# Kernel tuning notes

Hardware: AMD Instinct MI355X
Metric: run time of the kernel (lower is better)

Reference implementation:

```python
import jax, jax.numpy as jnp
import numpy as np

N, L, S = 2, 3000, 3000
C = 256          # in_depth
H = 256          # hidden_depth
FC = 8           # heads_count
SC_HID = H // FC # per-head dim of projected features
SCALE = (C // FC) ** 0.5  # torch code uses sc = in_depth // heads_count for scaling


def setup_inputs() -> dict:
    key = jax.random.key(0)
    ks = jax.random.split(key, 7)
    x0 = jax.random.normal(ks[0], (N, L, C), jnp.float32)
    x1 = jax.random.normal(ks[1], (N, S, C), jnp.float32)
    mask = jax.random.bernoulli(ks[2], 0.9, (N, L, S))
    W_proj = jax.random.normal(ks[3], (C, 2 * H), jnp.float32) / np.sqrt(C).astype(np.float32)
    b_proj = jax.random.normal(ks[4], (2 * H,), jnp.float32) * 0.01
    W_merge = jax.random.normal(ks[5], (H, C), jnp.float32) / np.sqrt(H).astype(np.float32)
    b_merge = jax.random.normal(ks[6], (C,), jnp.float32) * 0.01
    return {"x0": x0, "x1": x1, "mask": mask,
            "W_proj": W_proj, "b_proj": b_proj,
            "W_merge": W_merge, "b_merge": b_merge}


def _split_heads(x, W_proj, b_proj):
    # x: [n, t, C] -> proj [n, t, 2H] -> (qk, v) each [n, fc, t, sc]
    n, t, _ = x.shape
    p = (x @ W_proj + b_proj).reshape(n, t, 2, FC, SC_HID)  # layout (k fc sc)
    qk = jnp.transpose(p[:, :, 0], (0, 2, 1, 3))
    v = jnp.transpose(p[:, :, 1], (0, 2, 1, 3))
    return qk, v


def reference(x0, x1, mask, W_proj, b_proj, W_merge, b_merge):
    q0, v0 = _split_heads(x0, W_proj, b_proj)  # [n, f, l, d]
    q1, v1 = _split_heads(x1, W_proj, b_proj)  # [n, f, s, d]

    sim = jnp.einsum('nfld,nfsd->nfls', q0, q1)            # full score matrix
    sim = jnp.where(mask[:, None], sim, -jnp.inf) / SCALE  # mask then scale (as in torch)

    a01 = jnp.nan_to_num(jax.nn.softmax(sim, axis=3))  # rows over s
    a10 = jnp.nan_to_num(jax.nn.softmax(sim, axis=2))  # rows over l (== softmax(sim^T, -1))

    m0 = jnp.einsum('nfls,nfsd->nfld', a01, v1)  # [n, f, l, d]
    m1 = jnp.einsum('nfls,nfld->nfsd', a10, v0)  # [n, f, s, d]

    m0 = jnp.transpose(m0, (0, 2, 1, 3)).reshape(m0.shape[0], L, H) @ W_merge + b_merge
    m1 = jnp.transpose(m1, (0, 2, 1, 3)).reshape(m1.shape[0], S, H) @ W_merge + b_merge
    return m0, m1
```

## Files before the change

kernel.cpp:

```cpp
#include <hip/hip_runtime.h>
#include <cstdint>
#include <cstddef>

typedef unsigned int u32;
typedef unsigned short u16;
typedef uint8_t u8;
typedef unsigned long long u64;

constexpr int kNB = 2, kL = 3000, kS = 3000, kC = 256, kH = 256, kFC = 8, kD = 32;
constexpr int kTP = 3008;
constexpr int kMW = 48;
constexpr float kQSC = 0.5050097568f;

typedef __attribute__((ext_vector_type(8))) short short8;
typedef __attribute__((ext_vector_type(4))) float f32x4;

__device__ __forceinline__ u16 f2bf(float f) {
  u32 u = __float_as_uint(f);
  u += 0x7FFFu + ((u >> 16) & 1u);
  return (u16)(u >> 16);
}
__device__ __forceinline__ float bf2f(u16 h) { return __uint_as_float(((u32)h) << 16); }
__device__ __forceinline__ f32x4 mfma16(short8 a, short8 b, f32x4 c) {
  return __builtin_amdgcn_mfma_f32_16x16x32_bf16(a, b, c, 0, 0, 0);
}
__device__ __forceinline__ u32 pk2(float a, float b) {
  return (__float_as_uint(a) >> 16) | (__float_as_uint(b) & 0xFFFF0000u);
}
__device__ __forceinline__ float truncbf(float a) {
  return __uint_as_float(__float_as_uint(a) & 0xFFFF0000u);
}
__device__ __forceinline__ u32 bytes_nz(u32 w) {
  return ((w & 0xFFu) ? 1u : 0u) | (((w >> 8) & 0xFFu) ? 2u : 0u)
       | (((w >> 16) & 0xFFu) ? 4u : 0u) | ((w >> 24) ? 8u : 0u);
}
__device__ __forceinline__ u32 h2_nz(u32 w) {
  return ((w & 0xFFFFu) ? 1u : 0u) | ((w >> 16) ? 2u : 0u);
}

__device__ __forceinline__ u32 detect_mf_block(const u8* __restrict__ mraw,
                                               int tid, int* cnt) {
  if (tid < 8) cnt[tid] = 0;
  __syncthreads();
  uint4 mv = ((const uint4*)mraw)[tid];
  u32 wds[4] = {mv.x, mv.y, mv.z, mv.w};
  int l1[4] = {0,0,0,0}; int l3f1 = 0, l3c = 0;
#pragma unroll
  for (int k = 0; k < 4; ++k) {
    u32 wv = wds[k];
#pragma unroll
    for (int j = 0; j < 4; ++j) {
      u32 b = (wv >> (8 * j)) & 0xFFu;
      l1[j] += (b == 1u);
      if (j == 1) l3f1 += (b == 0x3Fu);
      if (j & 1) l3c += (b == 0x3Cu);
    }
  }
  if (l1[0]) atomicAdd(&cnt[0], l1[0]);
  if (l1[1]) atomicAdd(&cnt[1], l1[1]);
  if (l1[2]) atomicAdd(&cnt[2], l1[2]);
  if (l1[3]) atomicAdd(&cnt[3], l1[3]);
  if (l3f1)  atomicAdd(&cnt[4], l3f1);
  if (l3c)   atomicAdd(&cnt[5], l3c);
  __syncthreads();
  u32 mf;
  if (cnt[1] + cnt[2] + cnt[3] > 64) mf = 0;
  else if (cnt[0] > 64)              mf = 2;
  else if (cnt[4] > 64)              mf = 1;
  else if (cnt[5] > 64)              mf = 4;
  else                               mf = 3;
  return mf;
}
__device__ __forceinline__ u32 detect_f2_block(const u8* __restrict__ xraw,
                                               int tid, int* cnt) {
  if (tid == 0) cnt[0] = 0;
  __syncthreads();
  uint4 xv = ((const uint4*)xraw)[tid];
  u32 wds[4] = {xv.x, xv.y, xv.z, xv.w};
  int lex = 0;
#pragma unroll
  for (int k = 0; k < 4; ++k) {
    u32 b = (wds[k] >> 8) & 0x7Fu;
    lex += (b >= 0x3Eu && b <= 0x40u);
  }
  if (lex) atomicAdd(&cnt[0], lex);
  __syncthreads();
  return (cnt[0] > 300) ? 0u : 1u;
}

constexpr size_t SZ_Q   = (size_t)kNB * kFC * kTP * kD * 2;
constexpr size_t SZ_MH  = (size_t)kNB * kTP * kH * 2;
constexpr size_t SZ_XB  = (size_t)kNB * kL * kC * 2;
constexpr size_t SZ_MKB = (size_t)kNB * kMW * kTP * 8;
constexpr size_t OFF_Q0 = 256;
constexpr size_t OFF_Q1 = OFF_Q0 + SZ_Q;
constexpr size_t OFF_V0 = OFF_Q1 + SZ_Q;
constexpr size_t OFF_V1 = OFF_V0 + SZ_Q;
constexpr size_t OFF_M0 = OFF_V1 + SZ_Q;
constexpr size_t OFF_M1 = OFF_M0 + SZ_MH;
constexpr size_t OFF_WT = OFF_M1 + SZ_MH;
constexpr size_t OFF_WM = OFF_WT + (size_t)2 * kH * kC * 2;
constexpr size_t OFF_X0 = OFF_WM + (size_t)kC * kH * 2;
constexpr size_t OFF_X1 = OFF_X0 + SZ_XB;
constexpr size_t OFF_MKB  = OFF_X1 + SZ_XB;
constexpr size_t OFF_MKBT = OFF_MKB + SZ_MKB;

constexpr int NB_MASK = 47 * 47 * 2;
constexpr int NB_CVT  = 3000;
constexpr int NB_WT   = 2 * kH + kC;

__global__ __launch_bounds__(256) void k_prep(const void* __restrict__ mraw,
                                              const void* __restrict__ x0,
                                              const void* __restrict__ x1,
                                              const void* __restrict__ Wp,
                                              const void* __restrict__ Wm,
                                              u64* __restrict__ mkb, u64* __restrict__ mkbt,
                                              u16* __restrict__ xb0, u16* __restrict__ xb1,
                                              u16* __restrict__ WT, u16* __restrict__ WmT) {
  const int bx = blockIdx.x, tid = threadIdx.x;
  __shared__ int dcnt[8];
  if (bx < NB_MASK) {
    const u32 mf = detect_mf_block((const u8*)mraw, tid, dcnt);
    const int n = bx / 2209, r2 = bx % 2209;
    const int l0 = (r2 / 47) * 64, s0 = (r2 % 47) * 64;
    __shared__ u16 tb[64][4];
    {
      const int row = tid >> 2, sg = (tid & 3) * 16;
      const int l = l0 + row;
      u32 bits = 0;
      if (l < kL) {
        const size_t base = ((size_t)n * kL + l) * kS + s0 + sg;
        const bool full = (s0 + sg + 16 <= kS);
        if (mf == 3) {
          if (full) {
            const float4* p = (const float4*)(((const float*)mraw) + base);
            float4 a = p[0], b = p[1], c = p[2], d = p[3];
            bits = (u32)(a.x != 0.f)        | ((u32)(a.y != 0.f) << 1)
                 | ((u32)(a.z != 0.f) << 2) | ((u32)(a.w != 0.f) << 3)
                 | ((u32)(b.x != 0.f) << 4) | ((u32)(b.y != 0.f) << 5)
                 | ((u32)(b.z != 0.f) << 6) | ((u32)(b.w != 0.f) << 7)
                 | ((u32)(c.x != 0.f) << 8) | ((u32)(c.y != 0.f) << 9)
                 | ((u32)(c.z != 0.f) << 10)| ((u32)(c.w != 0.f) << 11)
                 | ((u32)(d.x != 0.f) << 12)| ((u32)(d.y != 0.f) << 13)
                 | ((u32)(d.z != 0.f) << 14)| ((u32)(d.w != 0.f) << 15);
          } else {
            for (int i = 0; i < 16; ++i)
              if (s0 + sg + i < kS && ((const float*)mraw)[base + i] != 0.f) bits |= 1u << i;
          }
        } else if (mf == 2) {
          if (full) {
            const uint4* p = (const uint4*)(((const u32*)mraw) + base);
            uint4 a = p[0], b = p[1], c = p[2], d = p[3];
            bits = (u32)(a.x != 0)        | ((u32)(a.y != 0) << 1)
                 | ((u32)(a.z != 0) << 2) | ((u32)(a.w != 0) << 3)
                 | ((u32)(b.x != 0) << 4) | ((u32)(b.y != 0) << 5)
                 | ((u32)(b.z != 0) << 6) | ((u32)(b.w != 0) << 7)
                 | ((u32)(c.x != 0) << 8) | ((u32)(c.y != 0) << 9)
                 | ((u32)(c.z != 0) << 10)| ((u32)(c.w != 0) << 11)
                 | ((u32)(d.x != 0) << 12)| ((u32)(d.y != 0) << 13)
                 | ((u32)(d.z != 0) << 14)| ((u32)(d.w != 0) << 15);
          } else {
            for (int i = 0; i < 16; ++i)
              if (s0 + sg + i < kS && ((const u32*)mraw)[base + i]) bits |= 1u << i;
          }
        } else if (mf == 0) {
          if (full) {
            const u8* m8 = (const u8*)mraw + base;
            uint2 a = *(const uint2*)(m8);
            uint2 b = *(const uint2*)(m8 + 8);
            bits = bytes_nz(a.x) | (bytes_nz(a.y) << 4)
                 | (bytes_nz(b.x) << 8) | (bytes_nz(b.y) << 12);
          } else {
            for (int i = 0; i < 16; ++i)
              if (s0 + sg + i < kS && ((const u8*)mraw)[base + i]) bits |= 1u << i;
          }
        } else {
          if (full) {
            const u16* m16 = (const u16*)mraw + base;
            uint4 a = *(const uint4*)(m16);
            uint4 b = *(const uint4*)(m16 + 8);
            bits = h2_nz(a.x) | (h2_nz(a.y) << 2) | (h2_nz(a.z) << 4) | (h2_nz(a.w) << 6)
                 | (h2_nz(b.x) << 8) | (h2_nz(b.y) << 10)
                 | (h2_nz(b.z) << 12) | (h2_nz(b.w) << 14);
          } else {
            for (int i = 0; i < 16; ++i)
              if (s0 + sg + i < kS && ((const u16*)mraw)[base + i]) bits |= 1u << i;
          }
        }
      }
      tb[row][tid & 3] = (u16)bits;
    }
    __syncthreads();
    const int w = tid >> 6, lane = tid & 63;
    for (int k = 0; k < 16; ++k) {
      const int ro = w * 16 + k;
      u32 b1 = (tb[ro][lane >> 4] >> (lane & 15)) & 1;
      u64 word = __ballot((int)b1);
      if (lane == 0) mkb[((size_t)n * kMW + (s0 >> 6)) * kTP + l0 + ro] = word;
      u32 b2 = (tb[lane][ro >> 4] >> (ro & 15)) & 1;
      u64 wordt = __ballot((int)b2);
      if (lane == 0) mkbt[((size_t)n * kMW + (l0 >> 6)) * kTP + s0 + ro] = wordt;
    }
  } else if (bx < NB_MASK + NB_CVT) {
    const u32 f2 = detect_f2_block((const u8*)x0, tid, dcnt);
    const int b2 = bx - NB_MASK;
    const void* X = (b2 >= 1500) ? x1 : x0;
    u16* B = (b2 >= 1500) ? xb1 : xb0;
    const int i = (b2 % 1500) * 256 + tid;
    if (f2 == 0) {
      ((uint2*)B)[i] = ((const uint2*)X)[i];
    } else {
      float4 v = ((const float4*)X)[i];
      uint2 o;
      o.x = (u32)f2bf(v.x) | ((u32)f2bf(v.y) << 16);
      o.y = (u32)f2bf(v.z) | ((u32)f2bf(v.w) << 16);
      ((uint2*)B)[i] = o;
    }
  } else {
    const u32 f2 = detect_f2_block((const u8*)x0, tid, dcnt);
    const int b = bx - NB_MASK - NB_CVT, k = tid;
    if (b < 2 * kH) {
      int col = b;
      u16 v = (f2 == 0) ? ((const u16*)Wp)[(size_t)k * (2 * kH) + col]
                        : f2bf(((const float*)Wp)[(size_t)k * (2 * kH) + col]);
      WT[(size_t)col * kC + k] = v;
    } else {
      int col = b - 2 * kH;
      u16 v = (f2 == 0) ? ((const u16*)Wm)[(size_t)k * kC + col]
                        : f2bf(((const float*)Wm)[(size_t)k * kC + col]);
      WmT[(size_t)col * kH + k] = v;
    }
  }
}

__global__ __launch_bounds__(256) void k_proj(const u16* __restrict__ xb0,
                                              const u16* __restrict__ xb1,
                                              const u16* __restrict__ WT,
                                              const void* __restrict__ bias,
                                              const void* __restrict__ x0raw,
                                              u16* __restrict__ q0, u16* __restrict__ v0t,
                                              u16* __restrict__ q1, u16* __restrict__ v1t) {
  __shared__ int dcnt[8];
  const int tid = threadIdx.x;
  const u32 f2 = detect_f2_block((const u8*)x0raw, tid, dcnt);
  const int z = blockIdx.z;
  const u16* X = z ? xb1 : xb0;
  u16* Q = z ? q1 : q0;
  u16* V = z ? v1t : v0t;
  const int w = tid >> 6, lane = tid & 63;
  const int quad = lane >> 4, c16 = lane & 15;
  const int rb = blockIdx.x, cb = blockIdx.y;

  __align__(16) __shared__ u16 sB[64 * 264];
  {
    const u16* wp = WT + (size_t)(cb * 64 + (tid >> 2)) * kC + (tid & 3) * 64;
    u16* sp = sB + (tid >> 2) * 264 + (tid & 3) * 64;
#pragma unroll
    for (int i = 0; i < 8; ++i) *(uint4*)(sp + i * 8) = *(const uint4*)(wp + i * 8);
  }
  __syncthreads();

  const int arow = rb * 64 + w * 16 + c16;
  const u16* ap = X + (size_t)arow * kC + quad * 8;
  f32x4 acc[4];
#pragma unroll
  for (int cg = 0; cg < 4; ++cg) acc[cg] = f32x4{0.f,0.f,0.f,0.f};
#pragma unroll
  for (int k0 = 0; k0 < 8; ++k0) {
    short8 a = *(const short8*)(ap + k0 * 32);
#pragma unroll
    for (int cg = 0; cg < 4; ++cg) {
      short8 b = *(const short8*)(sB + (cg * 16 + c16) * 264 + k0 * 32 + quad * 8);
      acc[cg] = mfma16(a, b, acc[cg]);
    }
  }

  const int row0 = rb * 64 + w * 16 + quad * 4;
  if (row0 < 6000) {
    const int n = (row0 >= kL) ? 1 : 0;
    const int t0 = row0 - n * kL;
#pragma unroll
    for (int cg = 0; cg < 4; ++cg) {
      const int c = cb * 64 + cg * 16 + c16;
      float bb = (f2 == 0) ? bf2f(((const u16*)bias)[c]) : ((const float*)bias)[c];
      if (c < kH) {
        int ff = c >> 5, d = c & 31;
        u16* qp = Q + ((size_t)(n * kFC + ff) * kTP + t0) * kD + d;
#pragma unroll
        for (int r = 0; r < 4; ++r) qp[(size_t)r * kD] = f2bf((acc[cg][r] + bb) * kQSC);
      } else {
        int cc = c - kH;
        int ff = cc >> 5, d = cc & 31;
        uint2 o;
        o.x = (u32)f2bf(acc[cg][0] + bb) | ((u32)f2bf(acc[cg][1] + bb) << 16);
        o.y = (u32)f2bf(acc[cg][2] + bb) | ((u32)f2bf(acc[cg][3] + bb) << 16);
        *(uint2*)(V + ((size_t)(n * kFC + ff) * kD + d) * kTP + t0) = o;
      }
    }
  }
}

__global__ __launch_bounds__(256) void k_flash(const u16* __restrict__ q0,
                                               const u16* __restrict__ q1,
                                               const u16* __restrict__ v0t,
                                               const u16* __restrict__ v1t,
                                               const u64* __restrict__ mkb,
                                               const u64* __restrict__ mkbt,
                                               u16* __restrict__ m0h, u16* __restrict__ m1h) {
  const int z = blockIdx.z;
  const u16* QA = z ? q1 : q0;
  const u16* QB = z ? q0 : q1;
  const u16* VT = z ? v0t : v1t;
  const u64* MB = z ? mkbt : mkb;
  u16* MO = z ? m1h : m0h;

  const int nf = blockIdx.y, n = nf >> 3, f = nf & 7;
  const int tid = threadIdx.x, w = tid >> 6, lane = tid & 63;
  const int quad = lane >> 4, c16 = lane & 15;

  __align__(16) __shared__ u16 sPall[4 * 4704];
  u16* sP = sPall + w * 4704;

  const u16* qa = QA + (size_t)(n * kFC + f) * kTP * kD;
  const u16* qb = QB + (size_t)(n * kFC + f) * kTP * kD;
  const u16* vt = VT + (size_t)(n * kFC + f) * kD * kTP;
  const u64* mb = MB + (size_t)n * kMW * kTP;

  const int l0 = blockIdx.x * 64;

  short8 af[4];
#pragma unroll
  for (int g = 0; g < 4; ++g) {
    const int ra = l0 + g * 16 + c16;
    af[g] = *(const short8*)(qa + (size_t)ra * kD + quad * 8);
  }

  f32x4 acc[4][2];
  float pSum[4];
#pragma unroll
  for (int g = 0; g < 4; ++g) {
    acc[g][0] = f32x4{0.f,0.f,0.f,0.f};
    acc[g][1] = f32x4{0.f,0.f,0.f,0.f};
    pSum[g] = 0.f;
  }

  u64 mword = mb[(size_t)w * kTP + l0 + lane];
  short8 aq0, aq1, aq2, aq3;
  {
    const u16* qbase = qb + (size_t)(w * 64 + c16) * kD + quad * 8;
    aq0 = *(const short8*)(qbase);
    aq1 = *(const short8*)(qbase + (size_t)16 * kD);
    aq2 = *(const short8*)(qbase + (size_t)32 * kD);
    aq3 = *(const short8*)(qbase + (size_t)48 * kD);
  }

#pragma unroll 1
  for (int jc = w; jc < 47; jc += 4) {
    const int j0 = jc * 64;
    const u16* vb = vt + (size_t)c16 * kTP + j0 + quad * 8;
    short8 bv00 = *(const short8*)(vb);
    short8 bv01 = *(const short8*)(vb + (size_t)16 * kTP);
    short8 bv10 = *(const short8*)(vb + 32);
    short8 bv11 = *(const short8*)(vb + (size_t)16 * kTP + 32);

    const u32 mlo = (u32)mword, mhi = (u32)(mword >> 32);

#pragma unroll
    for (int g = 0; g < 4; ++g) {
      const u32 lo = (u32)__shfl((int)mlo, g * 16 + c16);
      const u32 hi = (u32)__shfl((int)mhi, g * 16 + c16);
      float ps = 0.f;
#pragma unroll
      for (int t = 0; t < 4; ++t) {
        short8 aq = (t == 0) ? aq0 : (t == 1) ? aq1 : (t == 2) ? aq2 : aq3;
        f32x4 zz = {0.f,0.f,0.f,0.f};
        f32x4 s = mfma16(aq, af[g], zz);
        const u32 hh = (t & 2) ? hi : lo;
        const int base = (t & 1) * 16 + quad * 4;
        float p0 = ((hh >> (base + 0)) & 1) ? __builtin_amdgcn_exp2f(s[0]) : 0.f;
        float p1 = ((hh >> (base + 1)) & 1) ? __builtin_amdgcn_exp2f(s[1]) : 0.f;
        float p2 = ((hh >> (base + 2)) & 1) ? __builtin_amdgcn_exp2f(s[2]) : 0.f;
        float p3 = ((hh >> (base + 3)) & 1) ? __builtin_amdgcn_exp2f(s[3]) : 0.f;
        ps += (truncbf(p0) + truncbf(p1)) + (truncbf(p2) + truncbf(p3));
        uint2 pw; pw.x = pk2(p0, p1); pw.y = pk2(p2, p3);
        *(uint2*)(sP + (g * 16 + c16) * 72 + t * 16 + quad * 4) = pw;
      }
      pSum[g] += ps;
    }

    {
      int jn = jc + 4;
      const int jl = (jn < 47) ? jn : w;
      mword = mb[(size_t)jl * kTP + l0 + lane];
      const u16* qn = qb + (size_t)(jl * 64 + c16) * kD + quad * 8;
      aq0 = *(const short8*)(qn);
      aq1 = *(const short8*)(qn + (size_t)16 * kD);
      aq2 = *(const short8*)(qn + (size_t)32 * kD);
      aq3 = *(const short8*)(qn + (size_t)48 * kD);
    }

#pragma unroll
    for (int g = 0; g < 4; ++g) {
      short8 ap0 = *(const short8*)(sP + (g * 16 + c16) * 72 + quad * 8);
      short8 ap1 = *(const short8*)(sP + (g * 16 + c16) * 72 + 32 + quad * 8);
      acc[g][0] = mfma16(ap0, bv00, acc[g][0]);
      acc[g][1] = mfma16(ap0, bv01, acc[g][1]);
      acc[g][0] = mfma16(ap1, bv10, acc[g][0]);
      acc[g][1] = mfma16(ap1, bv11, acc[g][1]);
    }
  }

#pragma unroll
  for (int g = 0; g < 4; ++g) {
    float s = pSum[g];
    s += __shfl_xor(s, 16);
    s += __shfl_xor(s, 32);
    pSum[g] = s;
  }

  __syncthreads();
  float* buf = (float*)sPall;
  if (w > 0) {
    const int rbase = (w - 1) * 2304;
#pragma unroll
    for (int g = 0; g < 4; ++g) {
#pragma unroll
      for (int r = 0; r < 4; ++r) {
        buf[rbase + (g * 9 + r)     * 64 + lane] = acc[g][0][r];
        buf[rbase + (g * 9 + 4 + r) * 64 + lane] = acc[g][1][r];
      }
      buf[rbase + (g * 9 + 8) * 64 + lane] = pSum[g];
    }
  }
  __syncthreads();
  if (w == 0) {
#pragma unroll
    for (int g = 0; g < 4; ++g) {
      float lsum = pSum[g];
#pragma unroll
      for (int ww = 0; ww < 3; ++ww) lsum += buf[ww * 2304 + (g * 9 + 8) * 64 + lane];
#pragma unroll
      for (int r = 0; r < 4; ++r) {
        float n0 = acc[g][0][r], n1 = acc[g][1][r];
#pragma unroll
        for (int ww = 0; ww < 3; ++ww) {
          n0 += buf[ww * 2304 + (g * 9 + r)     * 64 + lane];
          n1 += buf[ww * 2304 + (g * 9 + 4 + r) * 64 + lane];
        }
        float ls = __shfl(lsum, quad * 4 + r);
        float rd = (ls > 0.f) ? (1.f / ls) : 0.f;
        int lrow = l0 + g * 16 + quad * 4 + r;
        if (lrow < kL) {
          size_t basep = ((size_t)n * kTP + lrow) * kH + f * kD;
          MO[basep + c16]      = f2bf(n0 * rd);
          MO[basep + 16 + c16] = f2bf(n1 * rd);
        }
      }
    }
  }
}

__global__ __launch_bounds__(256) void k_merge(const u16* __restrict__ m0h,
                                               const u16* __restrict__ m1h,
                                               const u16* __restrict__ WmT,
                                               const void* __restrict__ bias,
                                               const void* __restrict__ x0raw,
                                               void* __restrict__ out) {
  __shared__ int dcnt[8];
  const int tid = threadIdx.x;
  const u32 f2 = detect_f2_block((const u8*)x0raw, tid, dcnt);
  const int z = blockIdx.z;
  const u16* A = z ? m1h : m0h;
  const int w = tid >> 6, lane = tid & 63;
  const int quad = lane >> 4, c16 = lane & 15;
  const int rb = blockIdx.x, cb = blockIdx.y;

  __align__(16) __shared__ u16 sB[64 * 264];
  {
    const u16* wp = WmT + (size_t)(cb * 64 + (tid >> 2)) * kH + (tid & 3) * 64;
    u16* sp = sB + (tid >> 2) * 264 + (tid & 3) * 64;
#pragma unroll
    for (int i = 0; i < 8; ++i) *(uint4*)(sp + i * 8) = *(const uint4*)(wp + i * 8);
  }
  __syncthreads();

  const int arow = rb * 64 + w * 16 + c16;
  const u16* ap = A + (size_t)arow * kH + quad * 8;
  f32x4 acc[4];
#pragma unroll
  for (int cg = 0; cg < 4; ++cg) acc[cg] = f32x4{0.f,0.f,0.f,0.f};
#pragma unroll
  for (int k0 = 0; k0 < 8; ++k0) {
    short8 a = *(const short8*)(ap + k0 * 32);
#pragma unroll
    for (int cg = 0; cg < 4; ++cg) {
      short8 b = *(const short8*)(sB + (cg * 16 + c16) * 264 + k0 * 32 + quad * 8);
      acc[cg] = mfma16(a, b, acc[cg]);
    }
  }

  const int row0 = rb * 64 + w * 16 + quad * 4;
  const int n = (row0 >= kTP) ? 1 : 0;
  const int t0 = row0 - n * kTP;
  const size_t obase = (size_t)z * ((size_t)kNB * kL * kC);
#pragma unroll
  for (int cg = 0; cg < 4; ++cg) {
    const int c = cb * 64 + cg * 16 + c16;
    float bb = (f2 == 0) ? bf2f(((const u16*)bias)[c]) : ((const float*)bias)[c];
#pragma unroll
    for (int r = 0; r < 4; ++r) {
      const int t = t0 + r;
      if (t < kL) {
        size_t oi = obase + ((size_t)n * kL + t) * kC + c;
        float v = acc[cg][r] + bb;
        if (f2 == 0) ((u16*)out)[oi] = f2bf(v);
        else         ((float*)out)[oi] = v;
      }
    }
  }
}

extern "C" void kernel_launch(void* const* d_in, const int* in_sizes, int n_in,
                              void* d_out, int out_size, void* d_ws, size_t ws_size,
                              hipStream_t stream) {
  (void)in_sizes; (void)n_in; (void)out_size; (void)ws_size;
  u8* ws = (u8*)d_ws;
  u16* q0  = (u16*)(ws + OFF_Q0);
  u16* q1  = (u16*)(ws + OFF_Q1);
  u16* v0t = (u16*)(ws + OFF_V0);
  u16* v1t = (u16*)(ws + OFF_V1);
  u16* m0h = (u16*)(ws + OFF_M0);
  u16* m1h = (u16*)(ws + OFF_M1);
  u16* WT  = (u16*)(ws + OFF_WT);
  u16* WmT = (u16*)(ws + OFF_WM);
  u16* xb0 = (u16*)(ws + OFF_X0);
  u16* xb1 = (u16*)(ws + OFF_X1);
  u64* mkb  = (u64*)(ws + OFF_MKB);
  u64* mkbt = (u64*)(ws + OFF_MKBT);

  const void* x0 = d_in[0];
  const void* x1 = d_in[1];
  const void* mraw = d_in[2];
  const void* Wp = d_in[3];
  const void* bp = d_in[4];
  const void* Wm = d_in[5];
  const void* bm = d_in[6];

  k_prep<<<dim3(NB_MASK + NB_CVT + NB_WT), 256, 0, stream>>>(
      mraw, x0, x1, Wp, Wm, mkb, mkbt, xb0, xb1, WT, WmT);
  k_proj<<<dim3(94, 8, 2), 256, 0, stream>>>(xb0, xb1, WT, bp, x0, q0, v0t, q1, v1t);
  k_flash<<<dim3(47, 16, 2), 256, 0, stream>>>(q0, q1, v0t, v1t, mkb, mkbt, m0h, m1h);
  k_merge<<<dim3(94, 4, 2), 256, 0, stream>>>(m0h, m1h, WmT, bm, x0, d_out);
}
```

Measured before the change: 258.4 us.

## Fuse four kernels into one persistent kernel with grid-wide barriers

Replaces the four separate launches (prep, projection, flash attention, merge) with a single persistent kernel of 512 blocks. Each block loops over the virtual block indices of every stage, and atomic-counter grid barriers in the workspace separate the stages. This removes the launch gaps and tail idle time between kernels. In exchange it adds an extra memset, spin-wait barriers, and a fixed grid size that may cut occupancy or load balance for the flash stage; correctness also depends on all 512 blocks being resident at once.

```diff
diff --git a/kernel.cpp b/kernel.cpp
--- a/kernel.cpp
+++ b/kernel.cpp
@@ -10,6 +10,7 @@
 constexpr int kNB = 2, kL = 3000, kS = 3000, kC = 256, kH = 256, kFC = 8, kD = 32;
 constexpr int kTP = 3008;
 constexpr int kMW = 48;
+constexpr int kNBLK = 512;
 constexpr float kQSC = 0.5050097568f;
 
 typedef __attribute__((ext_vector_type(8))) short short8;
@@ -27,65 +28,12 @@
 __device__ __forceinline__ u32 pk2(float a, float b) {
   return (__float_as_uint(a) >> 16) | (__float_as_uint(b) & 0xFFFF0000u);
 }
-__device__ __forceinline__ float truncbf(float a) {
-  return __uint_as_float(__float_as_uint(a) & 0xFFFF0000u);
-}
 __device__ __forceinline__ u32 bytes_nz(u32 w) {
   return ((w & 0xFFu) ? 1u : 0u) | (((w >> 8) & 0xFFu) ? 2u : 0u)
        | (((w >> 16) & 0xFFu) ? 4u : 0u) | ((w >> 24) ? 8u : 0u);
 }
 __device__ __forceinline__ u32 h2_nz(u32 w) {
   return ((w & 0xFFFFu) ? 1u : 0u) | ((w >> 16) ? 2u : 0u);
-}
-
-__device__ __forceinline__ u32 detect_mf_block(const u8* __restrict__ mraw,
-                                               int tid, int* cnt) {
-  if (tid < 8) cnt[tid] = 0;
-  __syncthreads();
-  uint4 mv = ((const uint4*)mraw)[tid];
-  u32 wds[4] = {mv.x, mv.y, mv.z, mv.w};
-  int l1[4] = {0,0,0,0}; int l3f1 = 0, l3c = 0;
-#pragma unroll
-  for (int k = 0; k < 4; ++k) {
-    u32 wv = wds[k];
-#pragma unroll
-    for (int j = 0; j < 4; ++j) {
-      u32 b = (wv >> (8 * j)) & 0xFFu;
-      l1[j] += (b == 1u);
-      if (j == 1) l3f1 += (b == 0x3Fu);
-      if (j & 1) l3c += (b == 0x3Cu);
-    }
-  }
-  if (l1[0]) atomicAdd(&cnt[0], l1[0]);
-  if (l1[1]) atomicAdd(&cnt[1], l1[1]);
-  if (l1[2]) atomicAdd(&cnt[2], l1[2]);
-  if (l1[3]) atomicAdd(&cnt[3], l1[3]);
-  if (l3f1)  atomicAdd(&cnt[4], l3f1);
-  if (l3c)   atomicAdd(&cnt[5], l3c);
-  __syncthreads();
-  u32 mf;
-  if (cnt[1] + cnt[2] + cnt[3] > 64) mf = 0;
-  else if (cnt[0] > 64)              mf = 2;
-  else if (cnt[4] > 64)              mf = 1;
-  else if (cnt[5] > 64)              mf = 4;
-  else                               mf = 3;
-  return mf;
-}
-__device__ __forceinline__ u32 detect_f2_block(const u8* __restrict__ xraw,
-                                               int tid, int* cnt) {
-  if (tid == 0) cnt[0] = 0;
-  __syncthreads();
-  uint4 xv = ((const uint4*)xraw)[tid];
-  u32 wds[4] = {xv.x, xv.y, xv.z, xv.w};
-  int lex = 0;
-#pragma unroll
-  for (int k = 0; k < 4; ++k) {
-    u32 b = (wds[k] >> 8) & 0x7Fu;
-    lex += (b >= 0x3Eu && b <= 0x40u);
-  }
-  if (lex) atomicAdd(&cnt[0], lex);
-  __syncthreads();
-  return (cnt[0] > 300) ? 0u : 1u;
 }
 
 constexpr size_t SZ_Q   = (size_t)kNB * kFC * kTP * kD * 2;
@@ -105,418 +53,466 @@
 constexpr size_t OFF_MKB  = OFF_X1 + SZ_XB;
 constexpr size_t OFF_MKBT = OFF_MKB + SZ_MKB;
 
+__device__ __forceinline__ u32 detect_mf_block(const u8* __restrict__ mraw,
+                                               int tid, int* cnt) {
+  if (tid < 8) cnt[tid] = 0;
+  __syncthreads();
+  uint4 mv = ((const uint4*)mraw)[tid];
+  u32 wds[4] = {mv.x, mv.y, mv.z, mv.w};
+  int l1[4] = {0,0,0,0}; int l3f1 = 0, l3c = 0;
+#pragma unroll
+  for (int k = 0; k < 4; ++k) {
+    u32 wv = wds[k];
+#pragma unroll
+    for (int j = 0; j < 4; ++j) {
+      u32 b = (wv >> (8 * j)) & 0xFFu;
+      l1[j] += (b == 1u);
+      if (j == 1) l3f1 += (b == 0x3Fu);
+      if (j & 1) l3c += (b == 0x3Cu);
+    }
+  }
+  if (l1[0]) atomicAdd(&cnt[0], l1[0]);
+  if (l1[1]) atomicAdd(&cnt[1], l1[1]);
+  if (l1[2]) atomicAdd(&cnt[2], l1[2]);
+  if (l1[3]) atomicAdd(&cnt[3], l1[3]);
+  if (l3f1)  atomicAdd(&cnt[4], l3f1);
+  if (l3c)   atomicAdd(&cnt[5], l3c);
+  __syncthreads();
+  u32 mf;
+  if (cnt[1] + cnt[2] + cnt[3] > 64) mf = 0;
+  else if (cnt[0] > 64)              mf = 2;
+  else if (cnt[4] > 64)              mf = 1;
+  else if (cnt[5] > 64)              mf = 4;
+  else                               mf = 3;
+  return mf;
+}
+__device__ __forceinline__ u32 detect_f2_block(const u8* __restrict__ xraw,
+                                               int tid, int* cnt) {
+  __syncthreads();
+  if (tid == 0) cnt[6] = 0;
+  __syncthreads();
+  uint4 xv = ((const uint4*)xraw)[tid];
+  u32 wds[4] = {xv.x, xv.y, xv.z, xv.w};
+  int lex = 0;
+#pragma unroll
+  for (int k = 0; k < 4; ++k) {
+    u32 b = (wds[k] >> 8) & 0x7Fu;
+    lex += (b >= 0x3Eu && b <= 0x40u);
+  }
+  if (lex) atomicAdd(&cnt[6], lex);
+  __syncthreads();
+  return (cnt[6] > 300) ? 0u : 1u;
+}
+
+__device__ __forceinline__ void gridbar(u32* bar, int idx, int tid) {
+  __syncthreads();
+  if (tid == 0) {
+    __threadfence();
+    __hip_atomic_fetch_add(&bar[idx], 1u, __ATOMIC_ACQ_REL, __HIP_MEMORY_SCOPE_AGENT);
+    while (__hip_atomic_load(&bar[idx], __ATOMIC_ACQUIRE, __HIP_MEMORY_SCOPE_AGENT)
+           < (u32)kNBLK) { __builtin_amdgcn_s_sleep(2); }
+    __threadfence();
+  }
+  __syncthreads();
+}
+
 constexpr int NB_MASK = 47 * 47 * 2;
 constexpr int NB_CVT  = 3000;
 constexpr int NB_WT   = 2 * kH + kC;
-
-__global__ __launch_bounds__(256) void k_prep(const void* __restrict__ mraw,
-                                              const void* __restrict__ x0,
-                                              const void* __restrict__ x1,
-                                              const void* __restrict__ Wp,
-                                              const void* __restrict__ Wm,
-                                              u64* __restrict__ mkb, u64* __restrict__ mkbt,
-                                              u16* __restrict__ xb0, u16* __restrict__ xb1,
-                                              u16* __restrict__ WT, u16* __restrict__ WmT) {
-  const int bx = blockIdx.x, tid = threadIdx.x;
+constexpr int NB_PREP = NB_MASK + NB_CVT + NB_WT;
+constexpr int NB_PROJ = 94 * 8 * 2;
+constexpr int NB_FLSH = 47 * 16 * 2;
+constexpr int NB_MRG  = 94 * 4 * 2;
+
+__global__ __launch_bounds__(256, 2) void k_all(const void* __restrict__ mraw,
+                                                const void* __restrict__ x0,
+                                                const void* __restrict__ x1,
+                                                const void* __restrict__ Wp,
+                                                const void* __restrict__ Wm,
+                                                const void* __restrict__ bp,
+                                                const void* __restrict__ bm,
+                                                u8* __restrict__ ws,
+                                                void* __restrict__ out) {
+  u32* bar  = (u32*)ws;
+  u16* q0   = (u16*)(ws + OFF_Q0);
+  u16* q1   = (u16*)(ws + OFF_Q1);
+  u16* v0t  = (u16*)(ws + OFF_V0);
+  u16* v1t  = (u16*)(ws + OFF_V1);
+  u16* m0h  = (u16*)(ws + OFF_M0);
+  u16* m1h  = (u16*)(ws + OFF_M1);
+  u16* WT   = (u16*)(ws + OFF_WT);
+  u16* WmT  = (u16*)(ws + OFF_WM);
+  u16* xb0  = (u16*)(ws + OFF_X0);
+  u16* xb1  = (u16*)(ws + OFF_X1);
+  u64* mkb  = (u64*)(ws + OFF_MKB);
+  u64* mkbt = (u64*)(ws + OFF_MKBT);
+
+  const int bid = blockIdx.x, tid = threadIdx.x;
+  const int w = tid >> 6, lane = tid & 63;
+  const int quad = lane >> 4, c16 = lane & 15;
+
   __shared__ int dcnt[8];
-  if (bx < NB_MASK) {
-    const u32 mf = detect_mf_block((const u8*)mraw, tid, dcnt);
-    const int n = bx / 2209, r2 = bx % 2209;
-    const int l0 = (r2 / 47) * 64, s0 = (r2 % 47) * 64;
-    __shared__ u16 tb[64][4];
-    {
-      const int row = tid >> 2, sg = (tid & 3) * 16;
-      const int l = l0 + row;
-      u32 bits = 0;
-      if (l < kL) {
-        const size_t base = ((size_t)n * kL + l) * kS + s0 + sg;
-        const bool full = (s0 + sg + 16 <= kS);
-        if (mf == 3) {
-          if (full) {
-            const float4* p = (const float4*)(((const float*)mraw) + base);
-            float4 a = p[0], b = p[1], c = p[2], d = p[3];
-            bits = (u32)(a.x != 0.f)        | ((u32)(a.y != 0.f) << 1)
-                 | ((u32)(a.z != 0.f) << 2) | ((u32)(a.w != 0.f) << 3)
-                 | ((u32)(b.x != 0.f) << 4) | ((u32)(b.y != 0.f) << 5)
-                 | ((u32)(b.z != 0.f) << 6) | ((u32)(b.w != 0.f) << 7)
-                 | ((u32)(c.x != 0.f) << 8) | ((u32)(c.y != 0.f) << 9)
-                 | ((u32)(c.z != 0.f) << 10)| ((u32)(c.w != 0.f) << 11)
-                 | ((u32)(d.x != 0.f) << 12)| ((u32)(d.y != 0.f) << 13)
-                 | ((u32)(d.z != 0.f) << 14)| ((u32)(d.w != 0.f) << 15);
+  __align__(16) __shared__ u16 smem[4 * 4704];
+
+  const u32 mf = detect_mf_block((const u8*)mraw, tid, dcnt);
+  const u32 f2 = detect_f2_block((const u8*)x0, tid, dcnt);
+
+  for (int vb = bid; vb < NB_PREP; vb += kNBLK) {
+    if (vb < NB_MASK) {
+      const int n = vb / 2209, r2 = vb % 2209;
+      const int l0 = (r2 / 47) * 64, s0 = (r2 % 47) * 64;
+      u16 (*tb)[4] = (u16(*)[4])smem;
+      {
+        const int row = tid >> 2, sg = (tid & 3) * 16;
+        const int l = l0 + row;
+        u32 bits = 0;
+        if (l < kL) {
+          const size_t base = ((size_t)n * kL + l) * kS + s0 + sg;
+          const bool full = (s0 + sg + 16 <= kS);
+          if (mf == 3) {
+            if (full) {
+              const float4* p = (const float4*)(((const float*)mraw) + base);
+              float4 a = p[0], b = p[1], c = p[2], d = p[3];
+              bits = (u32)(a.x != 0.f)        | ((u32)(a.y != 0.f) << 1)
+                   | ((u32)(a.z != 0.f) << 2) | ((u32)(a.w != 0.f) << 3)
+                   | ((u32)(b.x != 0.f) << 4) | ((u32)(b.y != 0.f) << 5)
+                   | ((u32)(b.z != 0.f) << 6) | ((u32)(b.w != 0.f) << 7)
+                   | ((u32)(c.x != 0.f) << 8) | ((u32)(c.y != 0.f) << 9)
+                   | ((u32)(c.z != 0.f) << 10)| ((u32)(c.w != 0.f) << 11)
+                   | ((u32)(d.x != 0.f) << 12)| ((u32)(d.y != 0.f) << 13)
+                   | ((u32)(d.z != 0.f) << 14)| ((u32)(d.w != 0.f) << 15);
+            } else {
+              for (int i = 0; i < 16; ++i)
+                if (s0 + sg + i < kS && ((const float*)mraw)[base + i] != 0.f) bits |= 1u << i;
+            }
+          } else if (mf == 2) {
+            if (full) {
+              const uint4* p = (const uint4*)(((const u32*)mraw) + base);
+              uint4 a = p[0], b = p[1], c = p[2], d = p[3];
+              bits = (u32)(a.x != 0)        | ((u32)(a.y != 0) << 1)
+                   | ((u32)(a.z != 0) << 2) | ((u32)(a.w != 0) << 3)
+                   | ((u32)(b.x != 0) << 4) | ((u32)(b.y != 0) << 5)
+                   | ((u32)(b.z != 0) << 6) | ((u32)(b.w != 0) << 7)
+                   | ((u32)(c.x != 0) << 8) | ((u32)(c.y != 0) << 9)
+                   | ((u32)(c.z != 0) << 10)| ((u32)(c.w != 0) << 11)
+                   | ((u32)(d.x != 0) << 12)| ((u32)(d.y != 0) << 13)
+                   | ((u32)(d.z != 0) << 14)| ((u32)(d.w != 0) << 15);
+            } else {
+              for (int i = 0; i < 16; ++i)
+                if (s0 + sg + i < kS && ((const u32*)mraw)[base + i]) bits |= 1u << i;
+            }
+          } else if (mf == 0) {
+            if (full) {
+              const u8* m8 = (const u8*)mraw + base;
+              uint2 a = *(const uint2*)(m8);
+              uint2 b = *(const uint2*)(m8 + 8);
+              bits = bytes_nz(a.x) | (bytes_nz(a.y) << 4)
+                   | (bytes_nz(b.x) << 8) | (bytes_nz(b.y) << 12);
+            } else {
+              for (int i = 0; i < 16; ++i)
+                if (s0 + sg + i < kS && ((const u8*)mraw)[base + i]) bits |= 1u << i;
+            }
           } else {
-            for (int i = 0; i < 16; ++i)
-              if (s0 + sg + i < kS && ((const float*)mraw)[base + i] != 0.f) bits |= 1u << i;
-          }
-        } else if (mf == 2) {
-          if (full) {
-            const uint4* p = (const uint4*)(((const u32*)mraw) + base);
-            uint4 a = p[0], b = p[1], c = p[2], d = p[3];
-            bits = (u32)(a.x != 0)        | ((u32)(a.y != 0) << 1)
-                 | ((u32)(a.z != 0) << 2) | ((u32)(a.w != 0) << 3)
-                 | ((u32)(b.x != 0) << 4) | ((u32)(b.y != 0) << 5)
-                 | ((u32)(b.z != 0) << 6) | ((u32)(b.w != 0) << 7)
-                 | ((u32)(c.x != 0) << 8) | ((u32)(c.y != 0) << 9)
-                 | ((u32)(c.z != 0) << 10)| ((u32)(c.w != 0) << 11)
-                 | ((u32)(d.x != 0) << 12)| ((u32)(d.y != 0) << 13)
-                 | ((u32)(d.z != 0) << 14)| ((u32)(d.w != 0) << 15);
-          } else {
-            for (int i = 0; i < 16; ++i)
-              if (s0 + sg + i < kS && ((const u32*)mraw)[base + i]) bits |= 1u << i;
-          }
-        } else if (mf == 0) {
-          if (full) {
-            const u8* m8 = (const u8*)mraw + base;
-            uint2 a = *(const uint2*)(m8);
-            uint2 b = *(const uint2*)(m8 + 8);
-            bits = bytes_nz(a.x) | (bytes_nz(a.y) << 4)
-                 | (bytes_nz(b.x) << 8) | (bytes_nz(b.y) << 12);
-          } else {
-            for (int i = 0; i < 16; ++i)
-              if (s0 + sg + i < kS && ((const u8*)mraw)[base + i]) bits |= 1u << i;
-          }
-        } else {
-          if (full) {
-            const u16* m16 = (const u16*)mraw + base;
-            uint4 a = *(const uint4*)(m16);
-            uint4 b = *(const uint4*)(m16 + 8);
-            bits = h2_nz(a.x) | (h2_nz(a.y) << 2) | (h2_nz(a.z) << 4) | (h2_nz(a.w) << 6)
-                 | (h2_nz(b.x) << 8) | (h2_nz(b.y) << 10)
-                 | (h2_nz(b.z) << 12) | (h2_nz(b.w) << 14);
-          } else {
-            for (int i = 0; i < 16; ++i)
-              if (s0 + sg + i < kS && ((const u16*)mraw)[base + i]) bits |= 1u << i;
+            if (full) {
+              const u16* m16 = (const u16*)mraw + base;
+              uint4 a = *(const uint4*)(m16);
+              uint4 b = *(const uint4*)(m16 + 8);
+              bits = h2_nz(a.x) | (h2_nz(a.y) << 2) | (h2_nz(a.z) << 4) | (h2_nz(a.w) << 6)
+                   | (h2_nz(b.x) << 8) | (h2_nz(b.y) << 10)
+                   | (h2_nz(b.z) << 12) | (h2_nz(b.w) << 14);
+            } else {
+              for (int i = 0; i < 16; ++i)
+                if (s0 + sg + i < kS && ((const u16*)mraw)[base + i]) bits |= 1u << i;
+            }
           }
         }
-      }
-      tb[row][tid & 3] = (u16)bits;
-    }
-    __syncthreads();
-    const int w = tid >> 6, lane = tid & 63;
-    for (int k = 0; k < 16; ++k) {
-      const int ro = w * 16 + k;
-      u32 b1 = (tb[ro][lane >> 4] >> (lane & 15)) & 1;
-      u64 word = __ballot((int)b1);
-      if (lane == 0) mkb[((size_t)n * kMW + (s0 >> 6)) * kTP + l0 + ro] = word;
-      u32 b2 = (tb[lane][ro >> 4] >> (ro & 15)) & 1;
-      u64 wordt = __ballot((int)b2);
-      if (lane == 0) mkbt[((size_t)n * kMW + (l0 >> 6)) * kTP + s0 + ro] = wordt;
-    }
-  } else if (bx < NB_MASK + NB_CVT) {
-    const u32 f2 = detect_f2_block((const u8*)x0, tid, dcnt);
-    const int b2 = bx - NB_MASK;
-    const void* X = (b2 >= 1500) ? x1 : x0;
-    u16* B = (b2 >= 1500) ? xb1 : xb0;
-    const int i = (b2 % 1500) * 256 + tid;
-    if (f2 == 0) {
-      ((uint2*)B)[i] = ((const uint2*)X)[i];
+        tb[row][tid & 3] = (u16)bits;
+      }
+      __syncthreads();
+      for (int k = 0; k < 16; ++k) {
+        const int ro = w * 16 + k;
+        u32 b1 = (tb[ro][lane >> 4] >> (lane & 15)) & 1;
+        u64 word = __ballot((int)b1);
+        if (lane == 0) mkb[((size_t)n * kMW + (s0 >> 6)) * kTP + l0 + ro] = word;
+        u32 b2 = (tb[lane][ro >> 4] >> (ro & 15)) & 1;
+        u64 wordt = __ballot((int)b2);
+        if (lane == 0) mkbt[((size_t)n * kMW + (l0 >> 6)) * kTP + s0 + ro] = wordt;
+      }
+      __syncthreads();
+    } else if (vb < NB_MASK + NB_CVT) {
+      const int b2 = vb - NB_MASK;
+      const void* X = (b2 >= 1500) ? x1 : x0;
+      u16* B = (b2 >= 1500) ? xb1 : xb0;
+      const int i = (b2 % 1500) * 256 + tid;
+      if (f2 == 0) {
+        ((uint2*)B)[i] = ((const uint2*)X)[i];
+      } else {
+        float4 v = ((const float4*)X)[i];
+        uint2 o;
+        o.x = (u32)f2bf(v.x) | ((u32)f2bf(v.y) << 16);
+        o.y = (u32)f2bf(v.z) | ((u32)f2bf(v.w) << 16);
+        ((uint2*)B)[i] = o;
+      }
     } else {
-      float4 v = ((const float4*)X)[i];
-      uint2 o;
-      o.x = (u32)f2bf(v.x) | ((u32)f2bf(v.y) << 16);
-      o.y = (u32)f2bf(v.z) | ((u32)f2bf(v.w) << 16);
-      ((uint2*)B)[i] = o;
-    }
-  } else {
-    const u32 f2 = detect_f2_block((const u8*)x0, tid, dcnt);
-    const int b = bx - NB_MASK - NB_CVT, k = tid;
-    if (b < 2 * kH) {
-      int col = b;
-      u16 v = (f2 == 0) ? ((const u16*)Wp)[(size_t)k * (2 * kH) + col]
-                        : f2bf(((const float*)Wp)[(size_t)k * (2 * kH) + col]);
-      WT[(size_t)col * kC + k] = v;
-    } else {
-      int col = b - 2 * kH;
-      u16 v = (f2 == 0) ? ((const u16*)Wm)[(size_t)k * kC + col]
-                        : f2bf(((const float*)Wm)[(size_t)k * kC + col]);
-      WmT[(size_t)col * kH + k] = v;
-    }
-  }
-}
-
-__global__ __launch_bounds__(256) void k_proj(const u16* __restrict__ xb0,
-                                              const u16* __restrict__ xb1,
-                                              const u16* __restrict__ WT,
-                                              const void* __restrict__ bias,
-                                              const void* __restrict__ x0raw,
-                                              u16* __restrict__ q0, u16* __restrict__ v0t,
-                                              u16* __restrict__ q1, u16* __restrict__ v1t) {
-  __shared__ int dcnt[8];
-  const int tid = threadIdx.x;
-  const u32 f2 = detect_f2_block((const u8*)x0raw, tid, dcnt);
-  const int z = blockIdx.z;
-  const u16* X = z ? xb1 : xb0;
-  u16* Q = z ? q1 : q0;
-  u16* V = z ? v1t : v0t;
-  const int w = tid >> 6, lane = tid & 63;
-  const int quad = lane >> 4, c16 = lane & 15;
-  const int rb = blockIdx.x, cb = blockIdx.y;
-
-  __align__(16) __shared__ u16 sB[64 * 264];
-  {
-    const u16* wp = WT + (size_t)(cb * 64 + (tid >> 2)) * kC + (tid & 3) * 64;
-    u16* sp = sB + (tid >> 2) * 264 + (tid & 3) * 64;
-#pragma unroll
-    for (int i = 0; i < 8; ++i) *(uint4*)(sp + i * 8) = *(const uint4*)(wp + i * 8);
-  }
-  __syncthreads();
-
-  const int arow = rb * 64 + w * 16 + c16;
-  const u16* ap = X + (size_t)arow * kC + quad * 8;
-  f32x4 acc[4];
-#pragma unroll
-  for (int cg = 0; cg < 4; ++cg) acc[cg] = f32x4{0.f,0.f,0.f,0.f};
-#pragma unroll
-  for (int k0 = 0; k0 < 8; ++k0) {
-    short8 a = *(const short8*)(ap + k0 * 32);
-#pragma unroll
-    for (int cg = 0; cg < 4; ++cg) {
-      short8 b = *(const short8*)(sB + (cg * 16 + c16) * 264 + k0 * 32 + quad * 8);
-      acc[cg] = mfma16(a, b, acc[cg]);
-    }
-  }
-
-  const int row0 = rb * 64 + w * 16 + quad * 4;
-  if (row0 < 6000) {
-    const int n = (row0 >= kL) ? 1 : 0;
-    const int t0 = row0 - n * kL;
+      const int b = vb - NB_MASK - NB_CVT, k = tid;
+      if (b < 2 * kH) {
+        int col = b;
+        u16 v = (f2 == 0) ? ((const u16*)Wp)[(size_t)k * (2 * kH) + col]
+                          : f2bf(((const float*)Wp)[(size_t)k * (2 * kH) + col]);
+        WT[(size_t)col * kC + k] = v;
+      } else {
+        int col = b - 2 * kH;
+        u16 v = (f2 == 0) ? ((const u16*)Wm)[(size_t)k * kC + col]
+                          : f2bf(((const float*)Wm)[(size_t)k * kC + col]);
+        WmT[(size_t)col * kH + k] = v;
+      }
+    }
+  }
+  gridbar(bar, 0, tid);
+
+  for (int vb = bid; vb < NB_PROJ; vb += kNBLK) {
+    const int rb = vb % 94, cb = (vb / 94) % 8, z = vb / 752;
+    const u16* X = z ? xb1 : xb0;
+    u16* Q = z ? q1 : q0;
+    u16* V = z ? v1t : v0t;
+    u16* sB = smem;
+    {
+      const u16* wp = WT + (size_t)(cb * 64 + (tid >> 2)) * kC + (tid & 3) * 64;
+      u16* sp = sB + (tid >> 2) * 264 + (tid & 3) * 64;
+#pragma unroll
+      for (int i = 0; i < 8; ++i) *(uint4*)(sp + i * 8) = *(const uint4*)(wp + i * 8);
+    }
+    __syncthreads();
+
+    const int arow = rb * 64 + w * 16 + c16;
+    const u16* ap = X + (size_t)arow * kC + quad * 8;
+    f32x4 acc[4];
+#pragma unroll
+    for (int cg = 0; cg < 4; ++cg) acc[cg] = f32x4{0.f,0.f,0.f,0.f};
+#pragma unroll
+    for (int k0 = 0; k0 < 8; ++k0) {
+      short8 a = *(const short8*)(ap + k0 * 32);
+#pragma unroll
+      for (int cg = 0; cg < 4; ++cg) {
+        short8 b = *(const short8*)(sB + (cg * 16 + c16) * 264 + k0 * 32 + quad * 8);
+        acc[cg] = mfma16(a, b, acc[cg]);
+      }
+    }
+
+    const int row0 = rb * 64 + w * 16 + quad * 4;
+    if (row0 < 2 * kL) {
+      const int n = (row0 >= kL) ? 1 : 0;
+      const int t0 = row0 - n * kL;
+#pragma unroll
+      for (int cg = 0; cg < 4; ++cg) {
+        const int c = cb * 64 + cg * 16 + c16;
+        float bb = (f2 == 0) ? bf2f(((const u16*)bp)[c]) : ((const float*)bp)[c];
+        if (c < kH) {
+          int ff = c >> 5, d = c & 31;
+          u16* qp = Q + ((size_t)(n * kFC + ff) * kTP + t0) * kD + d;
+#pragma unroll
+          for (int r = 0; r < 4; ++r) qp[(size_t)r * kD] = f2bf((acc[cg][r] + bb) * kQSC);
+        } else {
+          int cc = c - kH;
+          int ff = cc >> 5, d = cc & 31;
+          uint2 o;
+          o.x = (u32)f2bf(acc[cg][0] + bb) | ((u32)f2bf(acc[cg][1] + bb) << 16);
+          o.y = (u32)f2bf(acc[cg][2] + bb) | ((u32)f2bf(acc[cg][3] + bb) << 16);
+          *(uint2*)(V + ((size_t)(n * kFC + ff) * kD + d) * kTP + t0) = o;
+        }
+      }
+    }
+    __syncthreads();
+  }
+  gridbar(bar, 1, tid);
+
+  for (int vb = bid; vb < NB_FLSH; vb += kNBLK) {
+    const int bx = vb % 47, nf = (vb / 47) % 16, z = vb / 752;
+    const u16* QA = z ? q1 : q0;
+    const u16* QB = z ? q0 : q1;
+    const u16* VT = z ? v0t : v1t;
+    const u64* MB = z ? mkbt : mkb;
+    u16* MO = z ? m1h : m0h;
+    const int n = nf >> 3, f = nf & 7;
+
+    u16* sP = smem + w * 4704;
+    const u16* qa = QA + (size_t)(n * kFC + f) * kTP * kD;
+    const u16* qb = QB + (size_t)(n * kFC + f) * kTP * kD;
+    const u16* vt = VT + (size_t)(n * kFC + f) * kD * kTP;
+    const u64* mb = MB + (size_t)n * kMW * kTP;
+    const int l0 = bx * 64;
+
+    short8 af[4];
+#pragma unroll
+    for (int g = 0; g < 4; ++g) {
+      const int ra = l0 + g * 16 + c16;
+      af[g] = *(const short8*)(qa + (size_t)ra * kD + quad * 8);
+    }
+    short8 bones;
+#pragma unroll
+    for (int i = 0; i < 8; ++i) bones[i] = (short)0x3F80;
+
+    f32x4 acc[4][2], accS[4];
+#pragma unroll
+    for (int g = 0; g < 4; ++g) {
+      acc[g][0] = f32x4{0.f,0.f,0.f,0.f};
+      acc[g][1] = f32x4{0.f,0.f,0.f,0.f};
+      accS[g]   = f32x4{0.f,0.f,0.f,0.f};
+    }
+
+    u64 mword = mb[(size_t)w * kTP + l0 + lane];
+    short8 aq0, aq1, aq2, aq3;
+    {
+      const u16* qbase = qb + (size_t)(w * 64 + c16) * kD + quad * 8;
+      aq0 = *(const short8*)(qbase);
+      aq1 = *(const short8*)(qbase + (size_t)16 * kD);
+      aq2 = *(const short8*)(qbase + (size_t)32 * kD);
+      aq3 = *(const short8*)(qbase + (size_t)48 * kD);
+    }
+
+#pragma unroll 1
+    for (int jc = w; jc < 47; jc += 4) {
+      const int j0 = jc * 64;
+      const u16* vbp = vt + (size_t)c16 * kTP + j0 + quad * 8;
+      short8 bv00 = *(const short8*)(vbp);
+      short8 bv01 = *(const short8*)(vbp + (size_t)16 * kTP);
+      short8 bv10 = *(const short8*)(vbp + 32);
+      short8 bv11 = *(const short8*)(vbp + (size_t)16 * kTP + 32);
+
+      const u32 mlo = (u32)mword, mhi = (u32)(mword >> 32);
+
+#pragma unroll
+      for (int g = 0; g < 4; ++g) {
+        const u32 lo = (u32)__shfl((int)mlo, g * 16 + c16);
+        const u32 hi = (u32)__shfl((int)mhi, g * 16 + c16);
+#pragma unroll
+        for (int t = 0; t < 4; ++t) {
+          short8 aq = (t == 0) ? aq0 : (t == 1) ? aq1 : (t == 2) ? aq2 : aq3;
+          f32x4 zz = {0.f,0.f,0.f,0.f};
+          f32x4 s = mfma16(aq, af[g], zz);
+          const u32 hh = (t & 2) ? hi : lo;
+          const int base = (t & 1) * 16 + quad * 4;
+          float p0 = ((hh >> (base + 0)) & 1) ? __builtin_amdgcn_exp2f(s[0]) : 0.f;
+          float p1 = ((hh >> (base + 1)) & 1) ? __builtin_amdgcn_exp2f(s[1]) : 0.f;
+          float p2 = ((hh >> (base + 2)) & 1) ? __builtin_amdgcn_exp2f(s[2]) : 0.f;
+          float p3 = ((hh >> (base + 3)) & 1) ? __builtin_amdgcn_exp2f(s[3]) : 0.f;
+          uint2 pw; pw.x = pk2(p0, p1); pw.y = pk2(p2, p3);
+          *(uint2*)(sP + (g * 16 + c16) * 72 + t * 16 + quad * 4) = pw;
+        }
+      }
+
+      {
+        int jn = jc + 4;
+        const int jl = (jn < 47) ? jn : w;
+        mword = mb[(size_t)jl * kTP + l0 + lane];
+        const u16* qn = qb + (size_t)(jl * 64 + c16) * kD + quad * 8;
+        aq0 = *(const short8*)(qn);
+        aq1 = *(const short8*)(qn + (size_t)16 * kD);
+        aq2 = *(const short8*)(qn + (size_t)32 * kD);
+        aq3 = *(const short8*)(qn + (size_t)48 * kD);
+      }
+
+#pragma unroll
+      for (int g = 0; g < 4; ++g) {
+        short8 ap0 = *(const short8*)(sP + (g * 16 + c16) * 72 + quad * 8);
+        short8 ap1 = *(const short8*)(sP + (g * 16 + c16) * 72 + 32 + quad * 8);
+        acc[g][0] = mfma16(ap0, bv00, acc[g][0]);
+        acc[g][1] = mfma16(ap0, bv01, acc[g][1]);
+        accS[g]   = mfma16(ap0, bones, accS[g]);
+        acc[g][0] = mfma16(ap1, bv10, acc[g][0]);
+        acc[g][1] = mfma16(ap1, bv11, acc[g][1]);
+        accS[g]   = mfma16(ap1, bones, accS[g]);
+      }
+    }
+
+    __syncthreads();
+    float* buf = (float*)smem;
+    if (w > 0) {
+      const int rbase = (w - 1) * 3072;
+#pragma unroll
+      for (int g = 0; g < 4; ++g) {
+#pragma unroll
+        for (int r = 0; r < 4; ++r) {
+          buf[rbase + (g * 12 + r)     * 64 + lane] = acc[g][0][r];
+          buf[rbase + (g * 12 + 4 + r) * 64 + lane] = acc[g][1][r];
+          buf[rbase + (g * 12 + 8 + r) * 64 + lane] = accS[g][r];
+        }
+      }
+    }
+    __syncthreads();
+    if (w == 0) {
+#pragma unroll
+      for (int g = 0; g < 4; ++g) {
+#pragma unroll
+        for (int r = 0; r < 4; ++r) {
+          float n0 = acc[g][0][r], n1 = acc[g][1][r], ls = accS[g][r];
+#pragma unroll
+          for (int ww = 0; ww < 3; ++ww) {
+            n0 += buf[ww * 3072 + (g * 12 + r)     * 64 + lane];
+            n1 += buf[ww * 3072 + (g * 12 + 4 + r) * 64 + lane];
+            ls += buf[ww * 3072 + (g * 12 + 8 + r) * 64 + lane];
+          }
+          float rd = (ls > 0.f) ? (1.f / ls) : 0.f;
+          int lrow = l0 + g * 16 + quad * 4 + r;
+          if (lrow < kL) {
+            size_t basep = ((size_t)n * kTP + lrow) * kH + f * kD;
+            MO[basep + c16]      = f2bf(n0 * rd);
+            MO[basep + 16 + c16] = f2bf(n1 * rd);
+          }
+        }
+      }
+    }
+    __syncthreads();
+  }
+  gridbar(bar, 2, tid);
+
+  for (int vb = bid; vb < NB_MRG; vb += kNBLK) {
+    const int rb = vb % 94, cb = (vb / 94) % 4, z = vb / 376;
+    const u16* A = z ? m1h : m0h;
+    u16* sB = smem;
+    {
+      const u16* wp = WmT + (size_t)(cb * 64 + (tid >> 2)) * kH + (tid & 3) * 64;
+      u16* sp = sB + (tid >> 2) * 264 + (tid & 3) * 64;
+#pragma unroll
+      for (int i = 0; i < 8; ++i) *(uint4*)(sp + i * 8) = *(const uint4*)(wp + i * 8);
+    }
+    __syncthreads();
+
+    const int arow = rb * 64 + w * 16 + c16;
+    const u16* ap = A + (size_t)arow * kH + quad * 8;
+    f32x4 acc[4];
+#pragma unroll
+    for (int cg = 0; cg < 4; ++cg) acc[cg] = f32x4{0.f,0.f,0.f,0.f};
+#pragma unroll
+    for (int k0 = 0; k0 < 8; ++k0) {
+      short8 a = *(const short8*)(ap + k0 * 32);
+#pragma unroll
+      for (int cg = 0; cg < 4; ++cg) {
+        short8 b = *(const short8*)(sB + (cg * 16 + c16) * 264 + k0 * 32 + quad * 8);
+        acc[cg] = mfma16(a, b, acc[cg]);
+      }
+    }
+
+    const int row0 = rb * 64 + w * 16 + quad * 4;
+    const int n = (row0 >= kTP) ? 1 : 0;
+    const int t0 = row0 - n * kTP;
+    const size_t obase = (size_t)z * ((size_t)kNB * kL * kC);
 #pragma unroll
     for (int cg = 0; cg < 4; ++cg) {
       const int c = cb * 64 + cg * 16 + c16;
-      float bb = (f2 == 0) ? bf2f(((const u16*)bias)[c]) : ((const float*)bias)[c];
-      if (c < kH) {
-        int ff = c >> 5, d = c & 31;
-        u16* qp = Q + ((size_t)(n * kFC + ff) * kTP + t0) * kD + d;
-#pragma unroll
-        for (int r = 0; r < 4; ++r) qp[(size_t)r * kD] = f2bf((acc[cg][r] + bb) * kQSC);
-      } else {
-        int cc = c - kH;
-        int ff = cc >> 5, d = cc & 31;
-        uint2 o;
-        o.x = (u32)f2bf(acc[cg][0] + bb) | ((u32)f2bf(acc[cg][1] + bb) << 16);
-        o.y = (u32)f2bf(acc[cg][2] + bb) | ((u32)f2bf(acc[cg][3] + bb) << 16);
-        *(uint2*)(V + ((size_t)(n * kFC + ff) * kD + d) * kTP + t0) = o;
-      }
-    }
-  }
-}
-
-__global__ __launch_bounds__(256) void k_flash(const u16* __restrict__ q0,
-                                               const u16* __restrict__ q1,
-                                               const u16* __restrict__ v0t,
-                                               const u16* __restrict__ v1t,
-                                               const u64* __restrict__ mkb,
-                                               const u64* __restrict__ mkbt,
-                                               u16* __restrict__ m0h, u16* __restrict__ m1h) {
-  const int z = blockIdx.z;
-  const u16* QA = z ? q1 : q0;
-  const u16* QB = z ? q0 : q1;
-  const u16* VT = z ? v0t : v1t;
-  const u64* MB = z ? mkbt : mkb;
-  u16* MO = z ? m1h : m0h;
-
-  const int nf = blockIdx.y, n = nf >> 3, f = nf & 7;
-  const int tid = threadIdx.x, w = tid >> 6, lane = tid & 63;
-  const int quad = lane >> 4, c16 = lane & 15;
-
-  __align__(16) __shared__ u16 sPall[4 * 4704];
-  u16* sP = sPall + w * 4704;
-
-  const u16* qa = QA + (size_t)(n * kFC + f) * kTP * kD;
-  const u16* qb = QB + (size_t)(n * kFC + f) * kTP * kD;
-  const u16* vt = VT + (size_t)(n * kFC + f) * kD * kTP;
-  const u64* mb = MB + (size_t)n * kMW * kTP;
-
-  const int l0 = blockIdx.x * 64;
-
-  short8 af[4];
-#pragma unroll
-  for (int g = 0; g < 4; ++g) {
-    const int ra = l0 + g * 16 + c16;
-    af[g] = *(const short8*)(qa + (size_t)ra * kD + quad * 8);
-  }
-
-  f32x4 acc[4][2];
-  float pSum[4];
-#pragma unroll
-  for (int g = 0; g < 4; ++g) {
-    acc[g][0] = f32x4{0.f,0.f,0.f,0.f};
-    acc[g][1] = f32x4{0.f,0.f,0.f,0.f};
-    pSum[g] = 0.f;
-  }
-
-  u64 mword = mb[(size_t)w * kTP + l0 + lane];
-  short8 aq0, aq1, aq2, aq3;
-  {
-    const u16* qbase = qb + (size_t)(w * 64 + c16) * kD + quad * 8;
-    aq0 = *(const short8*)(qbase);
-    aq1 = *(const short8*)(qbase + (size_t)16 * kD);
-    aq2 = *(const short8*)(qbase + (size_t)32 * kD);
-    aq3 = *(const short8*)(qbase + (size_t)48 * kD);
-  }
-
-#pragma unroll 1
-  for (int jc = w; jc < 47; jc += 4) {
-    const int j0 = jc * 64;
-    const u16* vb = vt + (size_t)c16 * kTP + j0 + quad * 8;
-    short8 bv00 = *(const short8*)(vb);
-    short8 bv01 = *(const short8*)(vb + (size_t)16 * kTP);
-    short8 bv10 = *(const short8*)(vb + 32);
-    short8 bv11 = *(const short8*)(vb + (size_t)16 * kTP + 32);
-
-    const u32 mlo = (u32)mword, mhi = (u32)(mword >> 32);
-
-#pragma unroll
-    for (int g = 0; g < 4; ++g) {
-      const u32 lo = (u32)__shfl((int)mlo, g * 16 + c16);
-      const u32 hi = (u32)__shfl((int)mhi, g * 16 + c16);
-      float ps = 0.f;
-#pragma unroll
-      for (int t = 0; t < 4; ++t) {
-        short8 aq = (t == 0) ? aq0 : (t == 1) ? aq1 : (t == 2) ? aq2 : aq3;
-        f32x4 zz = {0.f,0.f,0.f,0.f};
-        f32x4 s = mfma16(aq, af[g], zz);
-        const u32 hh = (t & 2) ? hi : lo;
-        const int base = (t & 1) * 16 + quad * 4;
-        float p0 = ((hh >> (base + 0)) & 1) ? __builtin_amdgcn_exp2f(s[0]) : 0.f;
-        float p1 = ((hh >> (base + 1)) & 1) ? __builtin_amdgcn_exp2f(s[1]) : 0.f;
-        float p2 = ((hh >> (base + 2)) & 1) ? __builtin_amdgcn_exp2f(s[2]) : 0.f;
-        float p3 = ((hh >> (base + 3)) & 1) ? __builtin_amdgcn_exp2f(s[3]) : 0.f;
-        ps += (truncbf(p0) + truncbf(p1)) + (truncbf(p2) + truncbf(p3));
-        uint2 pw; pw.x = pk2(p0, p1); pw.y = pk2(p2, p3);
-        *(uint2*)(sP + (g * 16 + c16) * 72 + t * 16 + quad * 4) = pw;
-      }
-      pSum[g] += ps;
-    }
-
-    {
-      int jn = jc + 4;
-      const int jl = (jn < 47) ? jn : w;
-      mword = mb[(size_t)jl * kTP + l0 + lane];
-      const u16* qn = qb + (size_t)(jl * 64 + c16) * kD + quad * 8;
-      aq0 = *(const short8*)(qn);
-      aq1 = *(const short8*)(qn + (size_t)16 * kD);
-      aq2 = *(const short8*)(qn + (size_t)32 * kD);
-      aq3 = *(const short8*)(qn + (size_t)48 * kD);
-    }
-
-#pragma unroll
-    for (int g = 0; g < 4; ++g) {
-      short8 ap0 = *(const short8*)(sP + (g * 16 + c16) * 72 + quad * 8);
-      short8 ap1 = *(const short8*)(sP + (g * 16 + c16) * 72 + 32 + quad * 8);
-      acc[g][0] = mfma16(ap0, bv00, acc[g][0]);
-      acc[g][1] = mfma16(ap0, bv01, acc[g][1]);
-      acc[g][0] = mfma16(ap1, bv10, acc[g][0]);
-      acc[g][1] = mfma16(ap1, bv11, acc[g][1]);
-    }
-  }
-
-#pragma unroll
-  for (int g = 0; g < 4; ++g) {
-    float s = pSum[g];
-    s += __shfl_xor(s, 16);
-    s += __shfl_xor(s, 32);
-    pSum[g] = s;
-  }
-
-  __syncthreads();
-  float* buf = (float*)sPall;
-  if (w > 0) {
-    const int rbase = (w - 1) * 2304;
-#pragma unroll
-    for (int g = 0; g < 4; ++g) {
+      float bb = (f2 == 0) ? bf2f(((const u16*)bm)[c]) : ((const float*)bm)[c];
 #pragma unroll
       for (int r = 0; r < 4; ++r) {
-        buf[rbase + (g * 9 + r)     * 64 + lane] = acc[g][0][r];
-        buf[rbase + (g * 9 + 4 + r) * 64 + lane] = acc[g][1][r];
-      }
-      buf[rbase + (g * 9 + 8) * 64 + lane] = pSum[g];
-    }
-  }
-  __syncthreads();
-  if (w == 0) {
-#pragma unroll
-    for (int g = 0; g < 4; ++g) {
-      float lsum = pSum[g];
-#pragma unroll
-      for (int ww = 0; ww < 3; ++ww) lsum += buf[ww * 2304 + (g * 9 + 8) * 64 + lane];
-#pragma unroll
-      for (int r = 0; r < 4; ++r) {
-        float n0 = acc[g][0][r], n1 = acc[g][1][r];
-#pragma unroll
-        for (int ww = 0; ww < 3; ++ww) {
-          n0 += buf[ww * 2304 + (g * 9 + r)     * 64 + lane];
-          n1 += buf[ww * 2304 + (g * 9 + 4 + r) * 64 + lane];
+        const int t = t0 + r;
+        if (t < kL) {
+          size_t oi = obase + ((size_t)n * kL + t) * kC + c;
+          float v = acc[cg][r] + bb;
+          if (f2 == 0) ((u16*)out)[oi] = f2bf(v);
+          else         ((float*)out)[oi] = v;
         }
-        float ls = __shfl(lsum, quad * 4 + r);
-        float rd = (ls > 0.f) ? (1.f / ls) : 0.f;
-        int lrow = l0 + g * 16 + quad * 4 + r;
-        if (lrow < kL) {
-          size_t basep = ((size_t)n * kTP + lrow) * kH + f * kD;
-          MO[basep + c16]      = f2bf(n0 * rd);
-          MO[basep + 16 + c16] = f2bf(n1 * rd);
-        }
-      }
-    }
-  }
-}
-
-__global__ __launch_bounds__(256) void k_merge(const u16* __restrict__ m0h,
-                                               const u16* __restrict__ m1h,
-                                               const u16* __restrict__ WmT,
-                                               const void* __restrict__ bias,
-                                               const void* __restrict__ x0raw,
-                                               void* __restrict__ out) {
-  __shared__ int dcnt[8];
-  const int tid = threadIdx.x;
-  const u32 f2 = detect_f2_block((const u8*)x0raw, tid, dcnt);
-  const int z = blockIdx.z;
-  const u16* A = z ? m1h : m0h;
-  const int w = tid >> 6, lane = tid & 63;
-  const int quad = lane >> 4, c16 = lane & 15;
-  const int rb = blockIdx.x, cb = blockIdx.y;
-
-  __align__(16) __shared__ u16 sB[64 * 264];
-  {
-    const u16* wp = WmT + (size_t)(cb * 64 + (tid >> 2)) * kH + (tid & 3) * 64;
-    u16* sp = sB + (tid >> 2) * 264 + (tid & 3) * 64;
-#pragma unroll
-    for (int i = 0; i < 8; ++i) *(uint4*)(sp + i * 8) = *(const uint4*)(wp + i * 8);
-  }
-  __syncthreads();
-
-  const int arow = rb * 64 + w * 16 + c16;
-  const u16* ap = A + (size_t)arow * kH + quad * 8;
-  f32x4 acc[4];
-#pragma unroll
-  for (int cg = 0; cg < 4; ++cg) acc[cg] = f32x4{0.f,0.f,0.f,0.f};
-#pragma unroll
-  for (int k0 = 0; k0 < 8; ++k0) {
-    short8 a = *(const short8*)(ap + k0 * 32);
-#pragma unroll
-    for (int cg = 0; cg < 4; ++cg) {
-      short8 b = *(const short8*)(sB + (cg * 16 + c16) * 264 + k0 * 32 + quad * 8);
-      acc[cg] = mfma16(a, b, acc[cg]);
-    }
-  }
-
-  const int row0 = rb * 64 + w * 16 + quad * 4;
-  const int n = (row0 >= kTP) ? 1 : 0;
-  const int t0 = row0 - n * kTP;
-  const size_t obase = (size_t)z * ((size_t)kNB * kL * kC);
-#pragma unroll
-  for (int cg = 0; cg < 4; ++cg) {
-    const int c = cb * 64 + cg * 16 + c16;
-    float bb = (f2 == 0) ? bf2f(((const u16*)bias)[c]) : ((const float*)bias)[c];
-#pragma unroll
-    for (int r = 0; r < 4; ++r) {
-      const int t = t0 + r;
-      if (t < kL) {
-        size_t oi = obase + ((size_t)n * kL + t) * kC + c;
-        float v = acc[cg][r] + bb;
-        if (f2 == 0) ((u16*)out)[oi] = f2bf(v);
-        else         ((float*)out)[oi] = v;
-      }
-    }
+      }
+    }
+    __syncthreads();
   }
 }
 
@@ -524,20 +520,6 @@
                               void* d_out, int out_size, void* d_ws, size_t ws_size,
                               hipStream_t stream) {
   (void)in_sizes; (void)n_in; (void)out_size; (void)ws_size;
-  u8* ws = (u8*)d_ws;
-  u16* q0  = (u16*)(ws + OFF_Q0);
-  u16* q1  = (u16*)(ws + OFF_Q1);
-  u16* v0t = (u16*)(ws + OFF_V0);
-  u16* v1t = (u16*)(ws + OFF_V1);
-  u16* m0h = (u16*)(ws + OFF_M0);
-  u16* m1h = (u16*)(ws + OFF_M1);
-  u16* WT  = (u16*)(ws + OFF_WT);
-  u16* WmT = (u16*)(ws + OFF_WM);
-  u16* xb0 = (u16*)(ws + OFF_X0);
-  u16* xb1 = (u16*)(ws + OFF_X1);
-  u64* mkb  = (u64*)(ws + OFF_MKB);
-  u64* mkbt = (u64*)(ws + OFF_MKBT);
-
   const void* x0 = d_in[0];
   const void* x1 = d_in[1];
   const void* mraw = d_in[2];
@@ -546,9 +528,7 @@
   const void* Wm = d_in[5];
   const void* bm = d_in[6];
 
-  k_prep<<<dim3(NB_MASK + NB_CVT + NB_WT), 256, 0, stream>>>(
-      mraw, x0, x1, Wp, Wm, mkb, mkbt, xb0, xb1, WT, WmT);
-  k_proj<<<dim3(94, 8, 2), 256, 0, stream>>>(xb0, xb1, WT, bp, x0, q0, v0t, q1, v1t);
-  k_flash<<<dim3(47, 16, 2), 256, 0, stream>>>(q0, q1, v0t, v1t, mkb, mkbt, m0h, m1h);
-  k_merge<<<dim3(94, 4, 2), 256, 0, stream>>>(m0h, m1h, WmT, bm, x0, d_out);
-}
+  hipMemsetAsync(d_ws, 0, 256, stream);
+  k_all<<<dim3(kNBLK), 256, 0, stream>>>(
+      mraw, x0, x1, Wp, Wm, bp, bm, (u8*)d_ws, d_out);
+}
```

Measured after the change: 519.3 us. 2.01x slower.
